# Optimization experiments

Hardware: AMD Instinct MI355X
Metric: run time of the kernel (lower is better)

Reference implementation:

```python
import jax, jax.numpy as jnp
import numpy as np

B, S, H, NH = 2, 2048, 4096, 32
D = H // NH  # head_dim = 128


def setup_inputs() -> dict:
    key = jax.random.key(0)
    ks = jax.random.split(key, 9)
    s = 1.0 / np.sqrt(H)
    return {
        "hidden_state": jax.random.normal(ks[0], (B, S, H), jnp.float32),
        "Wq": jax.random.normal(ks[1], (H, H), jnp.float32) * s,
        "bq": jax.random.normal(ks[2], (H,), jnp.float32) * 0.01,
        "Wk": jax.random.normal(ks[3], (D, H), jnp.float32) * s,
        "bk": jax.random.normal(ks[4], (D,), jnp.float32) * 0.01,
        "Wv": jax.random.normal(ks[5], (D, H), jnp.float32) * s,
        "bv": jax.random.normal(ks[6], (D,), jnp.float32) * 0.01,
        "Wo": jax.random.normal(ks[7], (H, H), jnp.float32) * s,
        "bo": jax.random.normal(ks[8], (H,), jnp.float32) * 0.01,
    }


def reference(hidden_state, Wq, bq, Wk, bk, Wv, bv, Wo, bo):
    b = hidden_state.shape[0]
    # Projections (torch Linear: x @ W.T + b)
    q = hidden_state @ Wq.T + bq              # (b, s, H)
    k = hidden_state @ Wk.T + bk              # (b, s, D) single shared KV head
    v = hidden_state @ Wv.T + bv              # (b, s, D)
    q = q.reshape(b, -1, NH, D).transpose(0, 2, 1, 3)  # (b, nh, s, d)
    # scores: broadcast the single K head across all query heads
    scale = 1.0 / jnp.sqrt(jnp.float32(D))
    scores = jnp.einsum("bhqd,bkd->bhqk", q, k) * scale   # (b, nh, s, s)
    probs = jax.nn.softmax(scores, axis=-1)
    out = jnp.einsum("bhqk,bkd->bhqd", probs, v)           # (b, nh, s, d)
    # Faithful to source: transpose(-1,-2) then view(b, -1, nh*d)
    out = jnp.swapaxes(out, -1, -2).reshape(b, -1, NH * D)  # (b, s, H) scrambled layout
    return out @ Wo.T + bo
```

## Files before the change

### kernel.cpp

```cpp
#include <hip/hip_runtime.h>
#include <hip/hip_bf16.h>

typedef __attribute__((ext_vector_type(8))) short bf16x8;
typedef __attribute__((ext_vector_type(4))) float f32x4;
typedef __attribute__((ext_vector_type(4))) unsigned int u32x4;
typedef __attribute__((ext_vector_type(2))) unsigned int u32x2;

__device__ __forceinline__ unsigned short f2bf(float f) {
    unsigned u = __builtin_bit_cast(unsigned, f);
    u += 0x7FFFu + ((u >> 16) & 1u);
    return (unsigned short)(u >> 16);
}

__device__ __forceinline__ void async16(const void* g, void* l) {
    __builtin_amdgcn_global_load_lds(
        (const __attribute__((address_space(1))) unsigned int*)g,
        (__attribute__((address_space(3))) unsigned int*)l, 16, 0, 0);
}

template <int N> __device__ __forceinline__ void waitv() {
    if constexpr (N == 8)      asm volatile("s_waitcnt vmcnt(8)" ::: "memory");
    else if constexpr (N == 6) asm volatile("s_waitcnt vmcnt(6)" ::: "memory");
    else if constexpr (N == 4) asm volatile("s_waitcnt vmcnt(4)" ::: "memory");
    else if constexpr (N == 3) asm volatile("s_waitcnt vmcnt(3)" ::: "memory");
    else                       asm volatile("s_waitcnt vmcnt(0)" ::: "memory");
}
#define BARF() do { __builtin_amdgcn_s_barrier(); asm volatile("" ::: "memory"); } while (0)

__device__ __forceinline__ void pl32(unsigned &a, unsigned &b) {
    u32x2 r = __builtin_amdgcn_permlane32_swap(a, b, false, false);
    a = r[0]; b = r[1];
}
__device__ __forceinline__ void pl16(unsigned &a, unsigned &b) {
    u32x2 r = __builtin_amdgcn_permlane16_swap(a, b, false, false);
    a = r[0]; b = r[1];
}

__global__ void cvt_f32_bf16(const float* __restrict__ x, unsigned short* __restrict__ y, int n4) {
    const int stride = gridDim.x * blockDim.x;
    for (int i = blockIdx.x * blockDim.x + threadIdx.x; i < n4; i += stride) {
        const float4 v = ((const float4*)x)[i];
        ushort4 o;
        o.x = f2bf(v.x); o.y = f2bf(v.y); o.z = f2bf(v.z); o.w = f2bf(v.w);
        ((ushort4*)y)[i] = o;
    }
}

template <int MREP, int MODE>
__global__ __launch_bounds__(512, 2) void gemm256(
    const unsigned short* __restrict__ A, const unsigned short* __restrict__ Bt,
    const float* __restrict__ b0, const float* __restrict__ b1, const float* __restrict__ b2,
    void* __restrict__ o0, unsigned short* __restrict__ o1, unsigned short* __restrict__ o2)
{
    constexpr int K = 4096, NT = 128;
    constexpr int ACALLS = MREP / 4;
    constexpr int CALLS  = ACALLS + 2;
    constexpr int ASH    = MREP * 1024;
    constexpr int SLOT   = ASH + 8192;
    __shared__ __align__(16) unsigned short lds[4 * SLOT];

    const int tid  = threadIdx.x;
    const int w    = tid >> 6, lane = tid & 63;
    const int l16  = lane & 15, quad = lane >> 4;
    const int wm   = w >> 2, wn = w & 3;

    int bx, by;
    {
        const int wg = (int)blockIdx.x;
        if constexpr (MODE == 1) {
            const int wgp = (wg & 7) * 68 + (wg >> 3);
            bx = wgp / 32; by = wgp % 32;
        } else {
            const int wgp = (wg & 7) * 32 + (wg >> 3);
            bx = wgp / 16; by = wgp % 16;
        }
    }
    const int m0 = by * (MREP * 32);
    const int n0 = bx * 256;

    const int srow = lane >> 2;
    const int schk = ((lane & 3) ^ ((lane >> 3) & 3)) * 8;
    const unsigned short* gAs[ACALLS];
#pragma unroll
    for (int c = 0; c < ACALLS; ++c)
        gAs[c] = A + (size_t)(m0 + (w * ACALLS + c) * 16 + srow) * K + schk;
    const unsigned short* gBs[2];
#pragma unroll
    for (int c = 0; c < 2; ++c)
        gBs[c] = Bt + (size_t)(n0 + (w * 2 + c) * 16 + srow) * K + schk;

    const int swz8 = (quad ^ ((l16 >> 1) & 3)) * 8;
    const int aoff = (wm * (MREP * 16) + l16) * 32 + swz8;
    const int boff = ASH + (wn * 64 + l16) * 32 + swz8;

    f32x4 acc[MREP][4] = {};

#define STAGE(tt) do { \
    unsigned short* lb = &lds[((tt) & 3) * SLOT]; \
    _Pragma("unroll") \
    for (int c = 0; c < ACALLS; ++c) \
        async16(gAs[c] + (tt) * 32, lb + (w * ACALLS + c) * 512); \
    _Pragma("unroll") \
    for (int c = 0; c < 2; ++c) \
        async16(gBs[c] + (tt) * 32, lb + ASH + (w * 2 + c) * 512); \
} while (0)

#define BODY(tt) do { \
    const unsigned short* lb = &lds[((tt) & 3) * SLOT]; \
    bf16x8 af[MREP], bfr[4]; \
    _Pragma("unroll") \
    for (int i = 0; i < MREP; ++i) af[i] = *(const bf16x8*)(lb + aoff + i * 512); \
    _Pragma("unroll") \
    for (int j = 0; j < 4; ++j)    bfr[j] = *(const bf16x8*)(lb + boff + j * 512); \
    __builtin_amdgcn_s_setprio(1); \
    _Pragma("unroll") \
    for (int i = 0; i < MREP; ++i) { \
        _Pragma("unroll") \
        for (int j = 0; j < 4; ++j) \
            acc[i][j] = __builtin_amdgcn_mfma_f32_16x16x32_bf16(af[i], bfr[j], acc[i][j], 0, 0, 0); \
    } \
    __builtin_amdgcn_s_setprio(0); \
} while (0)

    STAGE(0); STAGE(1); STAGE(2);
    for (int t = 0; t < NT - 3; ++t) {
        waitv<CALLS * 2>();
        BARF();
        STAGE(t + 3);
        BODY(t);
    }
    waitv<CALLS * 2>(); BARF(); BODY(NT - 3);
    waitv<CALLS>();     BARF(); BODY(NT - 2);
    waitv<0>();         BARF(); BODY(NT - 1);

#undef STAGE
#undef BODY

    if constexpr (MODE == 0) {
        float* C = (float*)o0;
#pragma unroll
        for (int j = 0; j < 4; ++j) {
            const int n = n0 + wn * 64 + j * 16 + l16;
            const float bb = b0[n];
#pragma unroll
            for (int i = 0; i < MREP; ++i) {
                const int mb = m0 + wm * (MREP * 16) + i * 16 + quad * 4;
#pragma unroll
                for (int r = 0; r < 4; ++r)
                    C[(size_t)(mb + r) * 4096 + n] = acc[i][j][r] + bb;
            }
        }
    } else {
        unsigned short* q_out = (unsigned short*)o0;
        const int nw0 = n0 + wn * 64;
        if (nw0 < 4096) {
#pragma unroll
            for (int j = 0; j < 4; ++j) {
                const int n = nw0 + j * 16 + l16;
                const float bb = b0[n];
#pragma unroll
                for (int i = 0; i < MREP; ++i) {
                    const int mb = m0 + wm * (MREP * 16) + i * 16 + quad * 4;
#pragma unroll
                    for (int r = 0; r < 4; ++r)
                        q_out[(size_t)(mb + r) * 4096 + n] = f2bf(acc[i][j][r] + bb);
                }
            }
        } else if (nw0 < 4224) {
#pragma unroll
            for (int j = 0; j < 4; ++j) {
                const int d = nw0 - 4096 + j * 16 + l16;
                const float bb = b1[d];
#pragma unroll
                for (int i = 0; i < MREP; ++i) {
                    const int mb = m0 + wm * (MREP * 16) + i * 16 + quad * 4;
#pragma unroll
                    for (int r = 0; r < 4; ++r)
                        o1[(size_t)(mb + r) * 128 + d] = f2bf(acc[i][j][r] + bb);
                }
            }
        } else {
#pragma unroll
            for (int j = 0; j < 4; ++j) {
                const int d = nw0 - 4224 + j * 16 + l16;
                const float bb = b2[d];
#pragma unroll
                for (int i = 0; i < MREP; ++i) {
                    const int mb = m0 + wm * (MREP * 16) + i * 16 + quad * 4;
                    ushort4 o;
                    o.x = f2bf(acc[i][j][0] + bb);
                    o.y = f2bf(acc[i][j][1] + bb);
                    o.z = f2bf(acc[i][j][2] + bb);
                    o.w = f2bf(acc[i][j][3] + bb);
                    *(ushort4*)(o2 + (size_t)((mb >> 11) * 128 + d) * 2048 + (mb & 2047)) = o;
                }
            }
        }
    }
}

__global__ __launch_bounds__(256) void attn_mqa(
    const unsigned short* __restrict__ Q,
    const unsigned short* __restrict__ Kb,
    const unsigned short* __restrict__ vT,
    unsigned short* __restrict__ scr)
{
    constexpr int S = 2048, D = 128, H = 4096;
    constexpr float CSC = 0.0883883476483184f * 1.4426950408889634f;

    __shared__ __align__(16) unsigned short lds[17536];

    const int tid = threadIdx.x;
    const int w = tid >> 6, lane = tid & 63;
    const int l16 = lane & 15, quad = lane >> 4;
    const int qb = blockIdx.x & 15;
    const int h  = (blockIdx.x >> 4) & 31;
    const int b  = blockIdx.x >> 9;
    const int q0 = qb * 128;

    bf16x8 qf[2][4];
#pragma unroll
    for (int mi = 0; mi < 2; ++mi)
#pragma unroll
        for (int ks = 0; ks < 4; ++ks)
            qf[mi][ks] = *(const bf16x8*)(Q + (size_t)(b * S + q0 + w * 32 + mi * 16 + l16) * H
                                            + h * D + ks * 32 + quad * 8);

    f32x4 Oa[2][8] = {};
    float l_run[2] = {};

    const unsigned short* gK = Kb + (size_t)(b * S + l16) * D + quad * 8;
    const unsigned short* gV = vT + (size_t)(b * 128 + l16) * 2048 + quad * 8;

    for (int kv0 = 0; kv0 < S; kv0 += 64) {
        __syncthreads();
#pragma unroll
        for (int t = 0; t < 4; ++t) {
            const int c = w * 4 + t;
            const int ct = c >> 2, ks = c & 3;
            async16(gK + (size_t)(kv0 + ct * 16) * D + ks * 32, &lds[c * 512]);
            const int nt = c >> 1, kk = c & 1;
            async16(gV + (size_t)(nt * 16) * 2048 + kv0 + kk * 32, &lds[8192 + c * 512]);
        }
        __syncthreads();

        f32x4 sf[2][4] = {};
#pragma unroll
        for (int ct = 0; ct < 4; ++ct)
#pragma unroll
            for (int ks = 0; ks < 4; ++ks) {
                const bf16x8 kf = *(const bf16x8*)&lds[(ct * 4 + ks) * 512 + lane * 8];
#pragma unroll
                for (int mi = 0; mi < 2; ++mi)
                    sf[mi][ct] = __builtin_amdgcn_mfma_f32_16x16x32_bf16(kf, qf[mi][ks], sf[mi][ct], 0, 0, 0);
            }

        bf16x8 pa[2][2];
#pragma unroll
        for (int mi = 0; mi < 2; ++mi) {
            unsigned cw[4][2];
#pragma unroll
            for (int ct = 0; ct < 4; ++ct) {
                const float p0 = exp2f(sf[mi][ct][0] * CSC);
                const float p1 = exp2f(sf[mi][ct][1] * CSC);
                const float p2 = exp2f(sf[mi][ct][2] * CSC);
                const float p3 = exp2f(sf[mi][ct][3] * CSC);
                l_run[mi] += (p0 + p1) + (p2 + p3);
                asm("v_cvt_pk_bf16_f32 %0, %1, %2" : "=v"(cw[ct][0]) : "v"(p0), "v"(p1));
                asm("v_cvt_pk_bf16_f32 %0, %1, %2" : "=v"(cw[ct][1]) : "v"(p2), "v"(p3));
            }
#pragma unroll
            for (int kk = 0; kk < 2; ++kk) {
                unsigned c0 = cw[2 * kk][0], c1 = cw[2 * kk][1];
                unsigned d0 = cw[2 * kk + 1][0], d1 = cw[2 * kk + 1][1];
                pl32(c0, d0); pl16(c0, d0);
                pl32(c1, d1); pl16(c1, d1);
                u32x4 t4; t4[0] = c0; t4[1] = c1; t4[2] = d0; t4[3] = d1;
                pa[mi][kk] = __builtin_bit_cast(bf16x8, t4);
            }
        }

#pragma unroll
        for (int nt = 0; nt < 8; ++nt)
#pragma unroll
            for (int kk = 0; kk < 2; ++kk) {
                const bf16x8 vf = *(const bf16x8*)&lds[8192 + (nt * 2 + kk) * 512 + lane * 8];
#pragma unroll
                for (int mi = 0; mi < 2; ++mi)
                    Oa[mi][nt] = __builtin_amdgcn_mfma_f32_16x16x32_bf16(pa[mi][kk], vf, Oa[mi][nt], 0, 0, 0);
            }
    }

    float iv[2][4];
#pragma unroll
    for (int mi = 0; mi < 2; ++mi) {
        float l = l_run[mi];
        l += __shfl_xor(l, 16);
        l += __shfl_xor(l, 32);
        const float linv = 1.f / l;
#pragma unroll
        for (int i = 0; i < 4; ++i)
            iv[mi][i] = __shfl(linv, quad * 4 + i);
    }

    __syncthreads();
#pragma unroll
    for (int mi = 0; mi < 2; ++mi)
#pragma unroll
        for (int nt = 0; nt < 8; ++nt)
#pragma unroll
            for (int i = 0; i < 4; ++i)
                lds[(nt * 16 + l16) * 136 + w * 32 + mi * 16 + quad * 4 + i] =
                    f2bf(Oa[mi][nt][i] * iv[mi][i]);
    __syncthreads();

    const int d = tid >> 1, qh = tid & 1;
    unsigned short* op = scr + (size_t)(b * S + h * 64 + (d >> 1)) * H + (d & 1) * 2048 + q0 + qh * 64;
#pragma unroll
    for (int j = 0; j < 8; ++j)
        *(int4*)(op + j * 8) = *(const int4*)&lds[d * 136 + qh * 64 + j * 8];
}

extern "C" void kernel_launch(void* const* d_in, const int* in_sizes, int n_in,
                              void* d_out, int out_size, void* d_ws, size_t ws_size,
                              hipStream_t stream) {
    (void)in_sizes; (void)n_in; (void)out_size; (void)ws_size;
    const float* hidden = (const float*)d_in[0];
    const float* Wq = (const float*)d_in[1];
    const float* bq = (const float*)d_in[2];
    const float* Wk = (const float*)d_in[3];
    const float* bk = (const float*)d_in[4];
    const float* Wv = (const float*)d_in[5];
    const float* bv = (const float*)d_in[6];
    const float* Wo = (const float*)d_in[7];
    const float* bo = (const float*)d_in[8];

    char* ws = (char*)d_ws;
    const size_t MB = 1048576;
    unsigned short* hb   = (unsigned short*)(ws);
    unsigned short* scr  = hb;
    unsigned short* Wcat = (unsigned short*)(ws + 32 * MB);
    unsigned short* Wob  = Wcat;
    unsigned short* q_b  = (unsigned short*)(ws + 68 * MB);
    unsigned short* k_b  = (unsigned short*)(ws + 100 * MB);
    unsigned short* vT   = (unsigned short*)(ws + 101 * MB);

    cvt_f32_bf16<<<1024, 256, 0, stream>>>(hidden, hb, 16777216 / 4);
    cvt_f32_bf16<<<1024, 256, 0, stream>>>(Wq, Wcat, 16777216 / 4);
    cvt_f32_bf16<<<256, 256, 0, stream>>>(Wk, Wcat + 16777216, 524288 / 4);
    cvt_f32_bf16<<<256, 256, 0, stream>>>(Wv, Wcat + 17301504, 524288 / 4);

    gemm256<4, 1><<<dim3(544), 512, 0, stream>>>(hb, Wcat, bq, bk, bv,
                                                 (void*)q_b, k_b, vT);
    cvt_f32_bf16<<<1024, 256, 0, stream>>>(Wo, Wob, 16777216 / 4);
    attn_mqa<<<1024, 256, 0, stream>>>(q_b, k_b, vT, scr);
    gemm256<8, 0><<<dim3(256), 512, 0, stream>>>(scr, Wob, bo, nullptr, nullptr,
                                                 (void*)d_out, nullptr, nullptr);
}
```

Measured before the change: 753.6 us.

## Double-buffer KV tiles in MQA attention with async prefetch and smaller tiles

Restructures the attention KV loop so each iteration works on a 32-key tile, and the next tile is prefetched into an alternate LDS buffer while the current one is computed. This replaces the two barriers per 64-key step with one wait plus one barrier per step. It also sets launch bounds to 4 blocks per CU and raises wave priority around the PV MFMA section. The price is twice as many loop iterations, each with less MFMA work, and a possible register pressure limit from the occupancy bound.

New measurement: 725.1 us. -3.8%, faster.

```diff
diff --git a/kernel.cpp b/kernel.cpp
--- a/kernel.cpp
+++ b/kernel.cpp
@@ -199,7 +199,7 @@
     }
 }
 
-__global__ __launch_bounds__(256) void attn_mqa(
+__global__ __launch_bounds__(256, 4) void attn_mqa(
     const unsigned short* __restrict__ Q,
     const unsigned short* __restrict__ Kb,
     const unsigned short* __restrict__ vT,
@@ -232,35 +232,43 @@
     const unsigned short* gK = Kb + (size_t)(b * S + l16) * D + quad * 8;
     const unsigned short* gV = vT + (size_t)(b * 128 + l16) * 2048 + quad * 8;
 
-    for (int kv0 = 0; kv0 < S; kv0 += 64) {
-        __syncthreads();
-#pragma unroll
-        for (int t = 0; t < 4; ++t) {
-            const int c = w * 4 + t;
-            const int ct = c >> 2, ks = c & 3;
-            async16(gK + (size_t)(kv0 + ct * 16) * D + ks * 32, &lds[c * 512]);
-            const int nt = c >> 1, kk = c & 1;
-            async16(gV + (size_t)(nt * 16) * 2048 + kv0 + kk * 32, &lds[8192 + c * 512]);
-        }
-        __syncthreads();
-
-        f32x4 sf[2][4] = {};
-#pragma unroll
-        for (int ct = 0; ct < 4; ++ct)
+#define ASTAGE(tt) do { \
+    unsigned short* buf = &lds[((tt) & 1) * 8192]; \
+    const int kv0s = (tt) * 32; \
+    _Pragma("unroll") \
+    for (int c2 = 0; c2 < 2; ++c2) { \
+        const int c = w * 2 + c2; \
+        async16(gK + (size_t)(kv0s + (c >> 2) * 16) * D + (c & 3) * 32, buf + c * 512); \
+        async16(gV + (size_t)(c * 16) * 2048 + kv0s, buf + 4096 + c * 512); \
+    } \
+} while (0)
+
+    ASTAGE(0);
+    for (int t = 0; t < 64; ++t) {
+        waitv<0>();
+        BARF();
+        if (t < 63) ASTAGE(t + 1);
+
+        const unsigned short* Kl = &lds[(t & 1) * 8192];
+        const unsigned short* Vl = Kl + 4096;
+
+        f32x4 sf[2][2] = {};
+#pragma unroll
+        for (int ct = 0; ct < 2; ++ct)
 #pragma unroll
             for (int ks = 0; ks < 4; ++ks) {
-                const bf16x8 kf = *(const bf16x8*)&lds[(ct * 4 + ks) * 512 + lane * 8];
+                const bf16x8 kf = *(const bf16x8*)&Kl[(ct * 4 + ks) * 512 + lane * 8];
 #pragma unroll
                 for (int mi = 0; mi < 2; ++mi)
                     sf[mi][ct] = __builtin_amdgcn_mfma_f32_16x16x32_bf16(kf, qf[mi][ks], sf[mi][ct], 0, 0, 0);
             }
 
-        bf16x8 pa[2][2];
+        bf16x8 pa[2];
 #pragma unroll
         for (int mi = 0; mi < 2; ++mi) {
-            unsigned cw[4][2];
-#pragma unroll
-            for (int ct = 0; ct < 4; ++ct) {
+            unsigned cw[2][2];
+#pragma unroll
+            for (int ct = 0; ct < 2; ++ct) {
                 const float p0 = exp2f(sf[mi][ct][0] * CSC);
                 const float p1 = exp2f(sf[mi][ct][1] * CSC);
                 const float p2 = exp2f(sf[mi][ct][2] * CSC);
@@ -269,27 +277,25 @@
                 asm("v_cvt_pk_bf16_f32 %0, %1, %2" : "=v"(cw[ct][0]) : "v"(p0), "v"(p1));
                 asm("v_cvt_pk_bf16_f32 %0, %1, %2" : "=v"(cw[ct][1]) : "v"(p2), "v"(p3));
             }
-#pragma unroll
-            for (int kk = 0; kk < 2; ++kk) {
-                unsigned c0 = cw[2 * kk][0], c1 = cw[2 * kk][1];
-                unsigned d0 = cw[2 * kk + 1][0], d1 = cw[2 * kk + 1][1];
-                pl32(c0, d0); pl16(c0, d0);
-                pl32(c1, d1); pl16(c1, d1);
-                u32x4 t4; t4[0] = c0; t4[1] = c1; t4[2] = d0; t4[3] = d1;
-                pa[mi][kk] = __builtin_bit_cast(bf16x8, t4);
-            }
-        }
-
-#pragma unroll
-        for (int nt = 0; nt < 8; ++nt)
-#pragma unroll
-            for (int kk = 0; kk < 2; ++kk) {
-                const bf16x8 vf = *(const bf16x8*)&lds[8192 + (nt * 2 + kk) * 512 + lane * 8];
-#pragma unroll
-                for (int mi = 0; mi < 2; ++mi)
-                    Oa[mi][nt] = __builtin_amdgcn_mfma_f32_16x16x32_bf16(pa[mi][kk], vf, Oa[mi][nt], 0, 0, 0);
-            }
-    }
+            unsigned c0 = cw[0][0], c1 = cw[0][1];
+            unsigned d0 = cw[1][0], d1 = cw[1][1];
+            pl32(c0, d0); pl16(c0, d0);
+            pl32(c1, d1); pl16(c1, d1);
+            u32x4 t4; t4[0] = c0; t4[1] = c1; t4[2] = d0; t4[3] = d1;
+            pa[mi] = __builtin_bit_cast(bf16x8, t4);
+        }
+
+        __builtin_amdgcn_s_setprio(1);
+#pragma unroll
+        for (int nt = 0; nt < 8; ++nt) {
+            const bf16x8 vf = *(const bf16x8*)&Vl[nt * 512 + lane * 8];
+#pragma unroll
+            for (int mi = 0; mi < 2; ++mi)
+                Oa[mi][nt] = __builtin_amdgcn_mfma_f32_16x16x32_bf16(pa[mi], vf, Oa[mi][nt], 0, 0, 0);
+        }
+        __builtin_amdgcn_s_setprio(0);
+    }
+#undef ASTAGE
 
     float iv[2][4];
 #pragma unroll
```
